# Performance work log

Measured on AMD Instinct MI355X. Metric: run time of the kernel, lower is better.

## Reference

```python
import jax, jax.numpy as jnp
import numpy as np
import math

B, C, H, W, S = 8, 512, 64, 64, 4


def setup_inputs() -> dict:
    key = jax.random.key(0)
    ks = jax.random.split(key, 7)
    s = 1.0 / math.sqrt(C)  # ~ torch Linear init scale
    x = jax.random.normal(ks[0], (B, C, H, W), jnp.float32)
    Wq = jax.random.uniform(ks[1], (C, C), jnp.float32, -s, s)
    bq = jax.random.uniform(ks[2], (C,), jnp.float32, -s, s)
    Wk = jax.random.uniform(ks[3], (C, C), jnp.float32, -s, s)
    bk = jax.random.uniform(ks[4], (C,), jnp.float32, -s, s)
    Wv = jax.random.uniform(ks[5], (C, C), jnp.float32, -s, s)
    bv = jax.random.uniform(ks[6], (C,), jnp.float32, -s, s)
    return {"x": x, "Wq": Wq, "bq": bq, "Wk": Wk, "bk": bk, "Wv": Wv, "bv": bv}


def reference(x, Wq, bq, Wk, bk, Wv, bv):
    # x: (B, C, H, W). Faithful to the torch module's output, but expressed
    # in the algebraically-equivalent efficient form: the repeat_interleaved
    # attention matrix A is block-constant, so out = repeat(A_m @ Vsum).
    b, c, h, w = x.shape
    nb = (h // S) * (w // S)  # number of SxS spatial blocks
    hw = h * w
    ss = S * S

    # Block means in unfold order (bh, bw): (B, nb, C)
    x_avg = x.reshape(b, c, h // S, S, w // S, S).mean(axis=(3, 5))
    x_avg = x_avg.reshape(b, c, nb).transpose(0, 2, 1)

    Q = x_avg @ Wq.T + bq  # (B, nb, C)
    K = x_avg @ Wk.T + bk  # (B, nb, C)
    A = jax.nn.softmax(jnp.einsum('bnc,bmc->bnm', Q, K) / jnp.sqrt(jnp.float32(c)), axis=-1)

    # V over flat row-major pixels: (B, HW, C)
    x_flat = x.reshape(b, c, hw).transpose(0, 2, 1)
    V = x_flat @ Wv.T + bv

    # repeat_interleave on dim=2 means column group j of A sums V rows
    # [j*ss, (j+1)*ss) in FLAT pixel order (not spatial blocks) - faithful.
    Vsum = V.reshape(b, hw // ss, ss, c).sum(axis=2)  # (B, nb, C)
    out_small = jnp.einsum('bnm,bmc->bnc', A, Vsum)   # (B, nb, C)
    # repeat_interleave on dim=1: each block row broadcast to ss flat pixels
    out_flat = jnp.repeat(out_small, ss, axis=1)      # (B, HW, C)
    return out_flat.transpose(0, 2, 1).reshape(b, c, h, w)
```

## Files before the change

kernel.cpp:

```cpp
#include <hip/hip_runtime.h>

typedef __attribute__((ext_vector_type(8))) short short8;
typedef __attribute__((ext_vector_type(4))) float f32x4;

__device__ __forceinline__ unsigned short f2bf(float f) {
    union { float f; unsigned int i; } v; v.f = f;
    unsigned int x = v.i;
    return (unsigned short)((x + 0x7FFFu + ((x >> 16) & 1u)) >> 16);
}
__device__ __forceinline__ f32x4 mfma16(short8 a, short8 b, f32x4 c) {
    return __builtin_amdgcn_mfma_f32_16x16x32_bf16(a, b, c, 0, 0, 0);
}

__global__ void prep_kernel(const float* __restrict__ x,
                            const float* __restrict__ Wq,
                            const float* __restrict__ Wk,
                            const float* __restrict__ Wv,
                            unsigned short* __restrict__ xavg,
                            unsigned short* __restrict__ xsum,
                            unsigned short* __restrict__ Wb)
{
    const int blk = blockIdx.x;
    const int t = threadIdx.x;
    if (blk >= 4096) {
        const int i = (blk - 4096) * 256 + t;
        const int m = i >> 15;
        const int o = (i & 32767) * 8;
        const float* src = (m == 0) ? Wq : (m == 1) ? Wk : Wv;
        unsigned short* dst = Wb + m * 262144 + o;
        float4 a = *(const float4*)(src + o);
        float4 b = *(const float4*)(src + o + 4);
        *(ushort4*)(dst)     = make_ushort4(f2bf(a.x), f2bf(a.y), f2bf(a.z), f2bf(a.w));
        *(ushort4*)(dst + 4) = make_ushort4(f2bf(b.x), f2bf(b.y), f2bf(b.z), f2bf(b.w));
        return;
    }
    const int b = blk >> 9;
    const int c = blk & 511;

    const float4* p = (const float4*)(x + (size_t)blk * 4096) + t * 4;
    float4 a0 = p[0], a1 = p[1], a2 = p[2], a3 = p[3];
    float s0 = a0.x + a0.y + a0.z + a0.w;
    float s1 = a1.x + a1.y + a1.z + a1.w;
    float s2 = a2.x + a2.y + a2.z + a2.w;
    float s3 = a3.x + a3.y + a3.z + a3.w;

    xsum[((size_t)b * 256 + t) * 512 + c] = f2bf(s0 + s1 + s2 + s3);

    __shared__ float part[1024];
    ((float4*)part)[t] = make_float4(s0, s1, s2, s3);
    __syncthreads();

    const int bh = t >> 4, bw = t & 15;
    float m = (part[(bh * 4 + 0) * 16 + bw] + part[(bh * 4 + 1) * 16 + bw] +
               part[(bh * 4 + 2) * 16 + bw] + part[(bh * 4 + 3) * 16 + bw]) * 0.0625f;
    xavg[((size_t)b * 256 + t) * 512 + c] = f2bf(m);
}

__global__ void __launch_bounds__(256, 2)
proj_gemm(const unsigned short* __restrict__ xavg,
          const unsigned short* __restrict__ xsum,
          const unsigned short* __restrict__ Wb,
          const float* __restrict__ bq,
          const float* __restrict__ bk,
          const float* __restrict__ bv,
          unsigned short* __restrict__ QK,
          unsigned short* __restrict__ VsT)
{
    const int blk = blockIdx.x;
    const int lane = threadIdx.x & 63, quad = lane >> 4, r16 = lane & 15;
    const int w = threadIdx.x >> 6;

    if (blk < 256) {
        const int wave = blk * 4 + w;
        const int mt2 = wave >> 4;
        const int nt4 = wave & 15;
        const unsigned short* xp0 = xavg + (size_t)(mt2 * 32 + r16) * 512 + quad * 8;
        const unsigned short* xp1 = xp0 + 16 * 512;
        const unsigned short* wp0 = Wb + (size_t)(nt4 * 64 + r16) * 512 + quad * 8;
        const unsigned short* wp1 = wp0 + 16 * 512;
        const unsigned short* wp2 = wp0 + 32 * 512;
        const unsigned short* wp3 = wp0 + 48 * 512;

        f32x4 a00 = {0,0,0,0}, a01 = a00, a02 = a00, a03 = a00;
        f32x4 a10 = a00, a11 = a00, a12 = a00, a13 = a00;
#pragma unroll 4
        for (int k = 0; k < 512; k += 32) {
            short8 qa0 = *(const short8*)(xp0 + k);
            short8 qa1 = *(const short8*)(xp1 + k);
            short8 b0 = *(const short8*)(wp0 + k);
            short8 b1 = *(const short8*)(wp1 + k);
            short8 b2 = *(const short8*)(wp2 + k);
            short8 b3 = *(const short8*)(wp3 + k);
            a00 = mfma16(qa0, b0, a00); a01 = mfma16(qa0, b1, a01);
            a02 = mfma16(qa0, b2, a02); a03 = mfma16(qa0, b3, a03);
            a10 = mfma16(qa1, b0, a10); a11 = mfma16(qa1, b1, a11);
            a12 = mfma16(qa1, b2, a12); a13 = mfma16(qa1, b3, a13);
        }
        const int row0 = mt2 * 32 + quad * 4;
        f32x4 accs0[4] = {a00, a01, a02, a03};
        f32x4 accs1[4] = {a10, a11, a12, a13};
#pragma unroll
        for (int j = 0; j < 4; ++j) {
            const int c = nt4 * 64 + j * 16 + r16;
            const float bias = (c < 512) ? bq[c] : bk[c - 512];
#pragma unroll
            for (int r = 0; r < 4; ++r) {
                QK[(size_t)(row0 + r) * 1024 + c]      = f2bf(accs0[j][r] + bias);
                QK[(size_t)(row0 + 16 + r) * 1024 + c] = f2bf(accs1[j][r] + bias);
            }
        }
    } else {
        const int vblk = blk - 256;
        const int b = vblk >> 4;
        const int wave = (vblk & 15) * 4 + w;
        const int mt2 = wave >> 3;
        const int nt4 = wave & 7;
        const unsigned short* xp0 = xsum + (size_t)b * 131072 + (size_t)(mt2 * 32 + r16) * 512 + quad * 8;
        const unsigned short* xp1 = xp0 + 16 * 512;
        const unsigned short* wp0 = Wb + 524288 + (size_t)(nt4 * 64 + r16) * 512 + quad * 8;
        const unsigned short* wp1 = wp0 + 16 * 512;
        const unsigned short* wp2 = wp0 + 32 * 512;
        const unsigned short* wp3 = wp0 + 48 * 512;

        f32x4 a00 = {0,0,0,0}, a01 = a00, a02 = a00, a03 = a00;
        f32x4 a10 = a00, a11 = a00, a12 = a00, a13 = a00;
#pragma unroll 4
        for (int k = 0; k < 512; k += 32) {
            short8 qa0 = *(const short8*)(xp0 + k);
            short8 qa1 = *(const short8*)(xp1 + k);
            short8 b0 = *(const short8*)(wp0 + k);
            short8 b1 = *(const short8*)(wp1 + k);
            short8 b2 = *(const short8*)(wp2 + k);
            short8 b3 = *(const short8*)(wp3 + k);
            a00 = mfma16(qa0, b0, a00); a01 = mfma16(qa0, b1, a01);
            a02 = mfma16(qa0, b2, a02); a03 = mfma16(qa0, b3, a03);
            a10 = mfma16(qa1, b0, a10); a11 = mfma16(qa1, b1, a11);
            a12 = mfma16(qa1, b2, a12); a13 = mfma16(qa1, b3, a13);
        }
        unsigned short* vb = VsT + (size_t)b * 131072;
        const int m0 = mt2 * 32 + quad * 4;
        f32x4 accs0[4] = {a00, a01, a02, a03};
        f32x4 accs1[4] = {a10, a11, a12, a13};
#pragma unroll
        for (int j = 0; j < 4; ++j) {
            const int c = nt4 * 64 + j * 16 + r16;
            const float bias = 16.f * bv[c];
#pragma unroll
            for (int r = 0; r < 4; ++r) {
                vb[(size_t)c * 256 + m0 + r]      = f2bf(accs0[j][r] + bias);
                vb[(size_t)c * 256 + m0 + 16 + r] = f2bf(accs1[j][r] + bias);
            }
        }
    }
}

__global__ void __launch_bounds__(256, 2)
attn_out(const unsigned short* __restrict__ QK,
         const unsigned short* __restrict__ VsT,
         float* __restrict__ out)
{
    __shared__ float S[32][257];
    __shared__ unsigned short Abf[32 * 264];
    float (*osT)[33] = (float(*)[33])&S[0][0];

    const int b = blockIdx.y;
    const int strip = blockIdx.x >> 3;
    const int cq = blockIdx.x & 7;
    const int w = threadIdx.x >> 6, lane = threadIdx.x & 63;
    const int quad = lane >> 4, r16 = lane & 15;

    {
        const unsigned short* qp0 = QK + (size_t)(b * 256 + strip * 32 + r16) * 1024 + quad * 8;
        const unsigned short* qp1 = qp0 + 16 * 1024;
        const unsigned short* kp0 = QK + (size_t)(b * 256 + w * 64 + r16) * 1024 + 512 + quad * 8;
        const unsigned short* kp1 = kp0 + 16 * 1024;
        const unsigned short* kp2 = kp0 + 32 * 1024;
        const unsigned short* kp3 = kp0 + 48 * 1024;

        f32x4 a00 = {0,0,0,0}, a01 = a00, a02 = a00, a03 = a00;
        f32x4 a10 = a00, a11 = a00, a12 = a00, a13 = a00;
#pragma unroll 4
        for (int k = 0; k < 512; k += 32) {
            short8 qa0 = *(const short8*)(qp0 + k);
            short8 qa1 = *(const short8*)(qp1 + k);
            short8 b0 = *(const short8*)(kp0 + k);
            short8 b1 = *(const short8*)(kp1 + k);
            short8 b2 = *(const short8*)(kp2 + k);
            short8 b3 = *(const short8*)(kp3 + k);
            a00 = mfma16(qa0, b0, a00); a01 = mfma16(qa0, b1, a01);
            a02 = mfma16(qa0, b2, a02); a03 = mfma16(qa0, b3, a03);
            a10 = mfma16(qa1, b0, a10); a11 = mfma16(qa1, b1, a11);
            a12 = mfma16(qa1, b2, a12); a13 = mfma16(qa1, b3, a13);
        }
        f32x4 accs0[4] = {a00, a01, a02, a03};
        f32x4 accs1[4] = {a10, a11, a12, a13};
#pragma unroll
        for (int j = 0; j < 4; ++j) {
            const int col = w * 64 + j * 16 + r16;
#pragma unroll
            for (int r = 0; r < 4; ++r) {
                S[quad * 4 + r][col]      = accs0[j][r];
                S[quad * 4 + 16 + r][col] = accs1[j][r];
            }
        }
    }
    __syncthreads();

    {
        const int t = threadIdx.x;
        const int r = t >> 3, seg = t & 7;
        float v[32];
        float mx = -3.4e38f;
#pragma unroll
        for (int j = 0; j < 32; ++j) {
            v[j] = S[r][seg * 32 + j] * 0.044194173824159216f;
            mx = fmaxf(mx, v[j]);
        }
        mx = fmaxf(mx, __shfl_xor(mx, 1));
        mx = fmaxf(mx, __shfl_xor(mx, 2));
        mx = fmaxf(mx, __shfl_xor(mx, 4));
        float sum = 0.f;
#pragma unroll
        for (int j = 0; j < 32; ++j) { v[j] = __expf(v[j] - mx); sum += v[j]; }
        sum += __shfl_xor(sum, 1);
        sum += __shfl_xor(sum, 2);
        sum += __shfl_xor(sum, 4);
        const float inv = 1.f / sum;
        unsigned short* ap = Abf + r * 264 + seg * 32;
#pragma unroll
        for (int j = 0; j < 32; j += 4)
            *(ushort4*)(ap + j) = make_ushort4(f2bf(v[j] * inv), f2bf(v[j + 1] * inv),
                                               f2bf(v[j + 2] * inv), f2bf(v[j + 3] * inv));
    }
    __syncthreads();

    {
        const int ch = w * 16 + r16;
        const unsigned short* ap0 = Abf + r16 * 264 + quad * 8;
        const unsigned short* ap1 = ap0 + 16 * 264;
        const unsigned short* vp  = VsT + (size_t)b * 131072 +
                                    (size_t)(cq * 64 + ch) * 256 + quad * 8;
        f32x4 acc0 = {0,0,0,0}, acc1 = acc0;
#pragma unroll
        for (int k = 0; k < 256; k += 32) {
            short8 a0 = *(const short8*)(ap0 + k);
            short8 a1 = *(const short8*)(ap1 + k);
            short8 b0 = *(const short8*)(vp + k);
            acc0 = mfma16(a0, b0, acc0);
            acc1 = mfma16(a1, b0, acc1);
        }
#pragma unroll
        for (int r = 0; r < 4; ++r) {
            osT[ch][quad * 4 + r]      = acc0[r];
            osT[ch][quad * 4 + 16 + r] = acc1[r];
        }
    }
    __syncthreads();

    {
        const int t = threadIdx.x;
        const int ch2 = t >> 7;
        const int j = t & 127;
        const int n = j >> 2;
        float* obase = out + (size_t)(b * 512 + cq * 64) * 4096 + strip * 512 + j * 4;
#pragma unroll
        for (int it = 0; it < 32; ++it) {
            const int ch = it * 2 + ch2;
            const float v = osT[ch][n];
            *(float4*)(obase + (size_t)ch * 4096) = make_float4(v, v, v, v);
        }
    }
}

extern "C" void kernel_launch(void* const* d_in, const int* in_sizes, int n_in,
                              void* d_out, int out_size, void* d_ws, size_t ws_size,
                              hipStream_t stream) {
    const float* x  = (const float*)d_in[0];
    const float* Wq = (const float*)d_in[1];
    const float* bq = (const float*)d_in[2];
    const float* Wk = (const float*)d_in[3];
    const float* bk = (const float*)d_in[4];
    const float* Wv = (const float*)d_in[5];
    const float* bv = (const float*)d_in[6];
    float* out = (float*)d_out;

    unsigned short* Wb   = (unsigned short*)d_ws;
    unsigned short* xavg = Wb + 786432;
    unsigned short* xsum = xavg + 1048576;
    unsigned short* QK   = xsum + 1048576;
    unsigned short* VsT  = QK + 2097152;

    prep_kernel<<<4480, 256, 0, stream>>>(x, Wq, Wk, Wv, xavg, xsum, Wb);
    proj_gemm<<<384, 256, 0, stream>>>(xavg, xsum, Wb, bq, bk, bv, QK, VsT);
    attn_out<<<dim3(64, 8), 256, 0, stream>>>(QK, VsT, out);
}
```

Before: 187.6 us.

## Split attention into shared score-softmax kernel and finer-grained AV expansion kernel

The fused attention kernel recomputed Q·K^T and softmax separately for each of eight channel groups. Scores and softmax are now computed once per row strip and stored as a bf16 matrix in workspace. A second kernel with smaller tiles and more blocks does A·Vsum and writes the broadcast output. This adds a kernel launch and a global round-trip for A, and the softmax kernel runs with only 64 blocks.

```diff
diff --git a/kernel.cpp b/kernel.cpp
--- a/kernel.cpp
+++ b/kernel.cpp
@@ -155,17 +155,11 @@
 }
 
 __global__ void __launch_bounds__(256, 2)
-attn_out(const unsigned short* __restrict__ QK,
-         const unsigned short* __restrict__ VsT,
-         float* __restrict__ out)
+score_softmax(const unsigned short* __restrict__ QK,
+              unsigned short* __restrict__ Amat)
 {
     __shared__ float S[32][257];
-    __shared__ unsigned short Abf[32 * 264];
-    float (*osT)[33] = (float(*)[33])&S[0][0];
-
-    const int b = blockIdx.y;
-    const int strip = blockIdx.x >> 3;
-    const int cq = blockIdx.x & 7;
+    const int b = blockIdx.y, strip = blockIdx.x;
     const int w = threadIdx.x >> 6, lane = threadIdx.x & 63;
     const int quad = lane >> 4, r16 = lane & 15;
 
@@ -226,46 +220,52 @@
         sum += __shfl_xor(sum, 2);
         sum += __shfl_xor(sum, 4);
         const float inv = 1.f / sum;
-        unsigned short* ap = Abf + r * 264 + seg * 32;
+        unsigned short* ap = Amat + (size_t)b * 65536 + (size_t)(strip * 32 + r) * 256 + seg * 32;
 #pragma unroll
         for (int j = 0; j < 32; j += 4)
             *(ushort4*)(ap + j) = make_ushort4(f2bf(v[j] * inv), f2bf(v[j + 1] * inv),
                                                f2bf(v[j + 2] * inv), f2bf(v[j + 3] * inv));
     }
+}
+
+__global__ void __launch_bounds__(256, 4)
+av_expand(const unsigned short* __restrict__ Amat,
+          const unsigned short* __restrict__ VsT,
+          float* __restrict__ out)
+{
+    __shared__ float osT[64][17];
+    const int b = blockIdx.y;
+    const int sh = blockIdx.x >> 3;
+    const int cq = blockIdx.x & 7;
+    const int w = threadIdx.x >> 6, lane = threadIdx.x & 63;
+    const int quad = lane >> 4, r16 = lane & 15;
+
+    {
+        const unsigned short* ap = Amat + (size_t)b * 65536 + (size_t)(sh * 16 + r16) * 256 + quad * 8;
+        const unsigned short* vp = VsT + (size_t)b * 131072 +
+                                   (size_t)(cq * 64 + w * 16 + r16) * 256 + quad * 8;
+        f32x4 acc = {0.f, 0.f, 0.f, 0.f};
+#pragma unroll
+        for (int k = 0; k < 256; k += 32) {
+            short8 a0 = *(const short8*)(ap + k);
+            short8 b0 = *(const short8*)(vp + k);
+            acc = mfma16(a0, b0, acc);
+        }
+#pragma unroll
+        for (int r = 0; r < 4; ++r)
+            osT[w * 16 + r16][quad * 4 + r] = acc[r];
+    }
     __syncthreads();
 
     {
-        const int ch = w * 16 + r16;
-        const unsigned short* ap0 = Abf + r16 * 264 + quad * 8;
-        const unsigned short* ap1 = ap0 + 16 * 264;
-        const unsigned short* vp  = VsT + (size_t)b * 131072 +
-                                    (size_t)(cq * 64 + ch) * 256 + quad * 8;
-        f32x4 acc0 = {0,0,0,0}, acc1 = acc0;
-#pragma unroll
-        for (int k = 0; k < 256; k += 32) {
-            short8 a0 = *(const short8*)(ap0 + k);
-            short8 a1 = *(const short8*)(ap1 + k);
-            short8 b0 = *(const short8*)(vp + k);
-            acc0 = mfma16(a0, b0, acc0);
-            acc1 = mfma16(a1, b0, acc1);
-        }
-#pragma unroll
-        for (int r = 0; r < 4; ++r) {
-            osT[ch][quad * 4 + r]      = acc0[r];
-            osT[ch][quad * 4 + 16 + r] = acc1[r];
-        }
-    }
-    __syncthreads();
-
-    {
         const int t = threadIdx.x;
-        const int ch2 = t >> 7;
-        const int j = t & 127;
+        const int ch4 = t >> 6;
+        const int j = t & 63;
         const int n = j >> 2;
-        float* obase = out + (size_t)(b * 512 + cq * 64) * 4096 + strip * 512 + j * 4;
-#pragma unroll
-        for (int it = 0; it < 32; ++it) {
-            const int ch = it * 2 + ch2;
+        float* obase = out + (size_t)(b * 512 + cq * 64) * 4096 + sh * 256 + j * 4;
+#pragma unroll
+        for (int it = 0; it < 16; ++it) {
+            const int ch = it * 4 + ch4;
             const float v = osT[ch][n];
             *(float4*)(obase + (size_t)ch * 4096) = make_float4(v, v, v, v);
         }
@@ -289,8 +289,10 @@
     unsigned short* xsum = xavg + 1048576;
     unsigned short* QK   = xsum + 1048576;
     unsigned short* VsT  = QK + 2097152;
+    unsigned short* Amat = VsT + 1048576;
 
     prep_kernel<<<4480, 256, 0, stream>>>(x, Wq, Wk, Wv, xavg, xsum, Wb);
     proj_gemm<<<384, 256, 0, stream>>>(xavg, xsum, Wb, bq, bk, bv, QK, VsT);
-    attn_out<<<dim3(64, 8), 256, 0, stream>>>(QK, VsT, out);
-}
+    score_softmax<<<dim3(8, 8), 256, 0, stream>>>(QK, Amat);
+    av_expand<<<dim3(128, 8), 256, 0, stream>>>(Amat, VsT, out);
+}
```

Result: faster. 182.1 us (-2.9%).
